# Performance work log

Hardware: AMD Instinct MI355X
Metric: run time of the kernel (lower is better)

## Reference

```python
import jax, jax.numpy as jnp
import numpy as np

N = 100000      # n_nodes
E = 1600000     # n_edges (avg degree 16)
F_IN = 128      # feat_dim
F_OUT = 128     # hid_dim


def setup_inputs() -> dict:
    key = jax.random.key(0)
    k1, k2, k3, k4 = jax.random.split(key, 4)
    x = jax.random.normal(k1, (N, F_IN), dtype=jnp.float32)
    edge_index = jax.random.randint(k2, (2, E), 0, N, dtype=jnp.int32)
    edge_weight = jax.random.uniform(k3, (E,), dtype=jnp.float32)
    # GCNConv level-0 parameters (Glorot-ish weight, zero bias as PyG default init)
    W = jax.random.normal(k4, (F_IN, F_OUT), dtype=jnp.float32) / np.sqrt(F_IN).astype(np.float32)
    b = jnp.zeros((F_OUT,), dtype=jnp.float32)
    return {"x": x, "W": W, "b": b, "level": 0,
            "edge_index": edge_index, "edge_weight": edge_weight}


def reference(x, W, b, level, edge_index, edge_weight):
    # PyG GCNConv: h = D^-1/2 (A + I) D^-1/2 (x @ W) + b ; Encoder also returns relu(h)
    n = x.shape[0]
    h = x @ W                                          # [N, F_OUT]
    src, dst = edge_index[0], edge_index[1]
    loop = jnp.arange(n, dtype=src.dtype)
    src = jnp.concatenate([src, loop])                 # add self-loops (weight 1)
    dst = jnp.concatenate([dst, loop])
    w = jnp.concatenate([edge_weight, jnp.ones((n,), edge_weight.dtype)])
    deg = jax.ops.segment_sum(w, dst, num_segments=n)  # in-degree by weight
    dinv = jnp.where(deg > 0, jax.lax.rsqrt(deg), 0.0)
    norm = dinv[src] * w * dinv[dst]                   # [E+N]
    emb = jax.ops.segment_sum(h[src] * norm[:, None], dst, num_segments=n) + b
    return emb, jax.nn.relu(emb)
```

## Files before the change

kernel.cpp:

```cpp
#include <hip/hip_runtime.h>

#define F 128
#define BSH 7
#define BWIDTH (1 << BSH)
#define MAX_NBKT 1024
#define CHUNK 4096
#define CAP 3072

typedef unsigned int uint;
typedef unsigned short ushort;

typedef __attribute__((ext_vector_type(8))) short bf16x8;
typedef __attribute__((ext_vector_type(4))) float f32x4;

union U4B8 { uint4 u; bf16x8 v; };

static __device__ inline ushort f2bf(float f) {
    uint u = __float_as_uint(f);
    return (ushort)((u + 0x7FFF + ((u >> 16) & 1)) >> 16);
}
static __device__ inline float bf2f(ushort h) {
    return __uint_as_float((uint)h << 16);
}

__global__ __launch_bounds__(256) void packW_kernel(const float* __restrict__ W,
                                                    uint4* __restrict__ wphi,
                                                    uint4* __restrict__ wplo,
                                                    int* __restrict__ gcur, int nbkt) {
    int idx = blockIdx.x * 256 + threadIdx.x;
    if (idx < nbkt) gcur[idx] = 0;
    if (idx >= 8 * 4 * 64) return;
    int l = idx & 63;
    int s = (idx >> 6) & 3;
    int t = idx >> 8;
    int p = t >> 1, q = t & 1;
    int col = 32 * p + 2 * (l & 15) + q;
    int kbase = 32 * s + (l >> 4) * 8;
    uint hi[8], lo[8];
    #pragma unroll
    for (int j = 0; j < 8; ++j) {
        float w = W[(size_t)(kbase + j) * F + col];
        ushort h = f2bf(w);
        lo[j] = f2bf(w - bf2f(h));
        hi[j] = h;
    }
    uint4 vh, vl;
    vh.x = hi[0] | (hi[1] << 16); vh.y = hi[2] | (hi[3] << 16);
    vh.z = hi[4] | (hi[5] << 16); vh.w = hi[6] | (hi[7] << 16);
    vl.x = lo[0] | (lo[1] << 16); vl.y = lo[2] | (lo[3] << 16);
    vl.z = lo[4] | (lo[5] << 16); vl.w = lo[6] | (lo[7] << 16);
    wphi[idx] = vh;
    wplo[idx] = vl;
}

__global__ __launch_bounds__(256) void scatter1_kernel(const int* __restrict__ src,
                                                       const int* __restrict__ dst,
                                                       const float* __restrict__ w,
                                                       int* __restrict__ gcur,
                                                       int2* __restrict__ ebuf,
                                                       int nbkt, int e) {
    __shared__ int hist[MAX_NBKT];
    __shared__ int cursor[MAX_NBKT];
    int t = threadIdx.x, blk = blockIdx.x;
    for (int i = t; i < nbkt; i += 256) hist[i] = 0;
    __syncthreads();
    int b0 = blk * CHUNK;
    #pragma unroll
    for (int j = 0; j < 16; ++j) {
        int i = b0 + t + 256 * j;
        if (i < e) atomicAdd(&hist[dst[i] >> BSH], 1);
    }
    __syncthreads();
    for (int i = t; i < nbkt; i += 256) {
        int c = hist[i];
        cursor[i] = c ? atomicAdd(&gcur[i], c) : 0;
    }
    __syncthreads();
    #pragma unroll
    for (int j = 0; j < 16; ++j) {
        int i = b0 + t + 256 * j;
        if (i < e) {
            int d = dst[i];
            int bk = d >> BSH;
            int pos = atomicAdd(&cursor[bk], 1);
            if (pos > CAP - 1) pos = CAP - 1;
            ebuf[(size_t)bk * CAP + pos] = make_int2(src[i] | ((d & (BWIDTH - 1)) << 17),
                                                     __float_as_int(w[i]));
        }
    }
}

__global__ __launch_bounds__(256) void bucket_build_kernel(int2* __restrict__ ebuf,
                                                           const int* __restrict__ gcur,
                                                           int2* __restrict__ rowinfo,
                                                           float* __restrict__ dinv,
                                                           int n, int nbkt) {
    __shared__ int2 stage[CAP];
    __shared__ int cnt[BWIDTH];
    __shared__ uint ws[BWIDTH];
    __shared__ float dvl[BWIDTH];
    __shared__ int cur[BWIDTH];
    __shared__ int offsh[BWIDTH];
    int b = blockIdx.x, t = threadIdx.x;
    size_t r0 = (size_t)b * CAP;
    int m = gcur[b];
    if (m > CAP) m = CAP;
    if (t < BWIDTH) { cnt[t] = 0; ws[t] = 0u; }
    __syncthreads();
    for (int i = t; i < m; i += 256) {
        int2 ed = ebuf[r0 + i];
        stage[i] = ed;
        int bl = (ed.x >> 17) & (BWIDTH - 1);
        atomicAdd(&cnt[bl], 1);
        atomicAdd(&ws[bl], (uint)(__int_as_float(ed.y) * 16777216.0f));
    }
    __syncthreads();
    if (t < BWIDTH) offsh[t] = cnt[t];
    __syncthreads();
    for (int off = 1; off < BWIDTH; off <<= 1) {
        int u = 0;
        if (t < BWIDTH && t >= off) u = offsh[t - off];
        __syncthreads();
        if (t < BWIDTH) offsh[t] += u;
        __syncthreads();
    }
    if (t < BWIDTH) {
        int excl = offsh[t] - cnt[t];
        cur[t] = excl;
        float dv = rsqrtf(1.0f + (float)ws[t] * (1.0f / 16777216.0f));
        dvl[t] = dv;
        int d = (b << BSH) + t;
        if (d < n) {
            rowinfo[d] = make_int2((int)(r0 + excl), cnt[t]);
            dinv[d] = dv;
        }
    }
    __syncthreads();
    for (int i = t; i < m; i += 256) {
        int2 ed = stage[i];
        int bl = (ed.x >> 17) & (BWIDTH - 1);
        int pos = atomicAdd(&cur[bl], 1);
        ebuf[r0 + pos] = make_int2(ed.x & 0x1FFFF,
                                   __float_as_int(__int_as_float(ed.y) * dvl[bl]));
    }
}

#define XPAD 136

__global__ __launch_bounds__(256) void gemm_kernel(const float* __restrict__ x,
                                                   const uint4* __restrict__ wphi,
                                                   const uint4* __restrict__ wplo,
                                                   ushort* __restrict__ hb, int n) {
    __shared__ ushort xhi[64][XPAD];
    __shared__ ushort xlo[64][XPAD];
    int row0 = blockIdx.x * 64;
    int t = threadIdx.x;
    #pragma unroll
    for (int i = 0; i < 8; ++i) {
        int v = t + 256 * i;
        int r = v >> 5, c4 = v & 31;
        int row = row0 + r;
        float4 val = (row < n) ? ((const float4*)x)[(size_t)row * 32 + c4]
                               : make_float4(0.f, 0.f, 0.f, 0.f);
        ushort h0 = f2bf(val.x), h1 = f2bf(val.y), h2 = f2bf(val.z), h3 = f2bf(val.w);
        ushort l0 = f2bf(val.x - bf2f(h0)), l1 = f2bf(val.y - bf2f(h1));
        ushort l2 = f2bf(val.z - bf2f(h2)), l3 = f2bf(val.w - bf2f(h3));
        *(ushort4*)&xhi[r][c4 * 4] = make_ushort4(h0, h1, h2, h3);
        *(ushort4*)&xlo[r][c4 * 4] = make_ushort4(l0, l1, l2, l3);
    }
    __syncthreads();

    int wv = t >> 6, l = t & 63;
    int m = l & 15, quad = l >> 4;
    f32x4 acc[8];
    #pragma unroll
    for (int i = 0; i < 8; ++i) acc[i] = (f32x4){0.f, 0.f, 0.f, 0.f};

    #pragma unroll
    for (int s = 0; s < 4; ++s) {
        bf16x8 ahi = *(const bf16x8*)&xhi[16 * wv + m][32 * s + quad * 8];
        bf16x8 alo = *(const bf16x8*)&xlo[16 * wv + m][32 * s + quad * 8];
        #pragma unroll
        for (int tt = 0; tt < 8; ++tt) {
            int widx = (tt * 4 + s) * 64 + l;
            U4B8 bh, bl;
            bh.u = wphi[widx];
            bl.u = wplo[widx];
            acc[tt] = __builtin_amdgcn_mfma_f32_16x16x32_bf16(ahi, bh.v, acc[tt], 0, 0, 0);
            acc[tt] = __builtin_amdgcn_mfma_f32_16x16x32_bf16(alo, bh.v, acc[tt], 0, 0, 0);
            acc[tt] = __builtin_amdgcn_mfma_f32_16x16x32_bf16(ahi, bl.v, acc[tt], 0, 0, 0);
        }
    }

    #pragma unroll
    for (int r = 0; r < 4; ++r) {
        int row = row0 + 16 * wv + quad * 4 + r;
        if (row < n) {
            uint* outp = (uint*)hb + (size_t)row * 64;
            #pragma unroll
            for (int p = 0; p < 4; ++p) {
                uint vp = (uint)f2bf(acc[2 * p][r]) | ((uint)f2bf(acc[2 * p + 1][r]) << 16);
                outp[p * 16 + m] = vp;
            }
        }
    }
}

__global__ __launch_bounds__(256) void aggregate_kernel(
        const ushort* __restrict__ hb, const int2* __restrict__ rowinfo,
        const int2* __restrict__ csr, const float* __restrict__ dinv,
        const float* __restrict__ b,
        float* __restrict__ out_emb, float* __restrict__ out_relu, int n) {
    int wave = threadIdx.x >> 6;
    int lane = threadIdx.x & 63;
    int i = blockIdx.x * 4 + wave;
    if (i >= n) return;
    int2 ri = rowinfo[i];
    int lo = ri.x, hi = ri.x + ri.y;
    float di = dinv[i];
    const uint* h32 = (const uint*)hb;
    uint hvu = h32[(size_t)i * 64 + lane];
    float2 bv = ((const float2*)b)[lane];
    float2 acc;
    acc.x = fmaf(__uint_as_float(hvu << 16) * di, di, bv.x);
    acc.y = fmaf(__uint_as_float(hvu & 0xFFFF0000u) * di, di, bv.y);
    for (int c = lo; c < hi; c += 64) {
        int m = min(64, hi - c);
        int sv = 0, nvi = 0;
        if (lane < m) {
            int2 en = csr[c + lane];
            sv = en.x;
            nvi = __float_as_int(__int_as_float(en.y) * dinv[sv]);
        }
        int mp = (m + 7) & ~7;
        for (int j = 0; j < mp; j += 8) {
            int ss[8]; float nw[8]; uint g[8];
            #pragma unroll
            for (int u = 0; u < 8; ++u) {
                ss[u] = __builtin_amdgcn_readlane(sv, j + u);
                nw[u] = __uint_as_float((uint)__builtin_amdgcn_readlane(nvi, j + u));
            }
            #pragma unroll
            for (int u = 0; u < 8; ++u)
                g[u] = h32[(size_t)ss[u] * 64 + lane];
            #pragma unroll
            for (int u = 0; u < 8; ++u) {
                acc.x = fmaf(__uint_as_float(g[u] << 16), nw[u], acc.x);
                acc.y = fmaf(__uint_as_float(g[u] & 0xFFFF0000u), nw[u], acc.y);
            }
        }
    }
    ((float2*)out_emb)[(size_t)i * 64 + lane] = acc;
    ((float2*)out_relu)[(size_t)i * 64 + lane] =
        make_float2(fmaxf(acc.x, 0.f), fmaxf(acc.y, 0.f));
}

extern "C" void kernel_launch(void* const* d_in, const int* in_sizes, int n_in,
                              void* d_out, int out_size, void* d_ws, size_t ws_size,
                              hipStream_t stream) {
    const float* x  = (const float*)d_in[0];
    const float* W  = (const float*)d_in[1];
    const float* b  = (const float*)d_in[2];
    const int*   ei = (const int*)d_in[4];
    const float* ew = (const float*)d_in[5];

    int n = in_sizes[0] / F;
    int e = in_sizes[4] / 2;
    const int* src = ei;
    const int* dst = ei + e;

    float* out_emb  = (float*)d_out;
    float* out_relu = out_emb + (size_t)n * F;

    int nbkt = (n + BWIDTH - 1) >> BSH;
    int eb   = (e + CHUNK - 1) / CHUNK;

    ushort* hb      = (ushort*)d_ws;
    int2*   ebuf    = (int2*)(hb + (size_t)n * F);
    uint4*  wphi    = (uint4*)(ebuf + (size_t)nbkt * CAP);
    uint4*  wplo    = wphi + 2048;
    int*    gcur    = (int*)(wplo + 2048);
    int2*   rowinfo = (int2*)(gcur + nbkt + 2);
    float*  dinv    = (float*)(rowinfo + n);

    packW_kernel<<<8, 256, 0, stream>>>(W, wphi, wplo, gcur, nbkt);
    scatter1_kernel<<<eb, 256, 0, stream>>>(src, dst, ew, gcur, ebuf, nbkt, e);
    bucket_build_kernel<<<nbkt, 256, 0, stream>>>(ebuf, gcur, rowinfo, dinv, n, nbkt);
    gemm_kernel<<<(n + 63) / 64, 256, 0, stream>>>(x, wphi, wplo, hb, n);
    aggregate_kernel<<<(n + 3) / 4, 256, 0, stream>>>(hb, rowinfo, ebuf, dinv, b,
                                                      out_emb, out_relu, n);
}
```

Before: 299.9 us.

## Locally sort edges per block before scattering and pad bucket counters

The edge scatter kernel now does a block-local counting sort in shared memory, with an exclusive scan over bucket histograms. It then writes edges to global memory in sorted order, so each bucket's writes are contiguous and coalesced rather than randomly scattered. Global bucket cursors are padded to 16 ints apart to reduce atomic contention and false sharing. The chunk is halved to 2048 edges to fit the shared staging buffers, which doubles the number of blocks and the count of global atomics.

```diff
diff --git a/kernel.cpp b/kernel.cpp
--- a/kernel.cpp
+++ b/kernel.cpp
@@ -4,8 +4,9 @@
 #define BSH 7
 #define BWIDTH (1 << BSH)
 #define MAX_NBKT 1024
-#define CHUNK 4096
+#define CHUNK 2048
 #define CAP 3072
+#define GPAD 16
 
 typedef unsigned int uint;
 typedef unsigned short ushort;
@@ -28,7 +29,7 @@
                                                     uint4* __restrict__ wplo,
                                                     int* __restrict__ gcur, int nbkt) {
     int idx = blockIdx.x * 256 + threadIdx.x;
-    if (idx < nbkt) gcur[idx] = 0;
+    for (int z = idx; z < nbkt * GPAD; z += 2048) gcur[z] = 0;
     if (idx >= 8 * 4 * 64) return;
     int l = idx & 63;
     int s = (idx >> 6) & 3;
@@ -60,34 +61,69 @@
                                                        int2* __restrict__ ebuf,
                                                        int nbkt, int e) {
     __shared__ int hist[MAX_NBKT];
+    __shared__ int shift[MAX_NBKT];
     __shared__ int cursor[MAX_NBKT];
+    __shared__ int2 sorted[CHUNK];
+    __shared__ int outaddr[CHUNK];
+    __shared__ int scanbuf[256];
     int t = threadIdx.x, blk = blockIdx.x;
     for (int i = t; i < nbkt; i += 256) hist[i] = 0;
     __syncthreads();
     int b0 = blk * CHUNK;
-    #pragma unroll
-    for (int j = 0; j < 16; ++j) {
+    int mtot = min(CHUNK, e - b0);
+    #pragma unroll
+    for (int j = 0; j < 8; ++j) {
         int i = b0 + t + 256 * j;
         if (i < e) atomicAdd(&hist[dst[i] >> BSH], 1);
     }
     __syncthreads();
-    for (int i = t; i < nbkt; i += 256) {
-        int c = hist[i];
-        cursor[i] = c ? atomicAdd(&gcur[i], c) : 0;
-    }
-    __syncthreads();
-    #pragma unroll
-    for (int j = 0; j < 16; ++j) {
+    int b4 = t * 4;
+    int h0 = 0, h1 = 0, h2 = 0, h3 = 0;
+    if (b4 < nbkt)     h0 = hist[b4];
+    if (b4 + 1 < nbkt) h1 = hist[b4 + 1];
+    if (b4 + 2 < nbkt) h2 = hist[b4 + 2];
+    if (b4 + 3 < nbkt) h3 = hist[b4 + 3];
+    int sum = h0 + h1 + h2 + h3;
+    scanbuf[t] = sum;
+    __syncthreads();
+    for (int off = 1; off < 256; off <<= 1) {
+        int u = (t >= off) ? scanbuf[t - off] : 0;
+        __syncthreads();
+        scanbuf[t] += u;
+        __syncthreads();
+    }
+    int excl = scanbuf[t] - sum;
+    int ls[4] = { excl, excl + h0, excl + h0 + h1, excl + h0 + h1 + h2 };
+    int hs[4] = { h0, h1, h2, h3 };
+    #pragma unroll
+    for (int q = 0; q < 4; ++q) {
+        int i = b4 + q;
+        if (i < nbkt) {
+            int c = hs[q];
+            int res = c ? atomicAdd(&gcur[i * GPAD], c) : 0;
+            cursor[i] = ls[q];
+            shift[i] = i * CAP + res - ls[q];
+        }
+    }
+    __syncthreads();
+    #pragma unroll
+    for (int j = 0; j < 8; ++j) {
         int i = b0 + t + 256 * j;
         if (i < e) {
             int d = dst[i];
             int bk = d >> BSH;
             int pos = atomicAdd(&cursor[bk], 1);
-            if (pos > CAP - 1) pos = CAP - 1;
-            ebuf[(size_t)bk * CAP + pos] = make_int2(src[i] | ((d & (BWIDTH - 1)) << 17),
-                                                     __float_as_int(w[i]));
-        }
-    }
+            int a = shift[bk] + pos;
+            int amax = bk * CAP + (CAP - 1);
+            if (a > amax) a = amax;
+            sorted[pos] = make_int2(src[i] | ((d & (BWIDTH - 1)) << 17),
+                                    __float_as_int(w[i]));
+            outaddr[pos] = a;
+        }
+    }
+    __syncthreads();
+    for (int i = t; i < mtot; i += 256)
+        ebuf[outaddr[i]] = sorted[i];
 }
 
 __global__ __launch_bounds__(256) void bucket_build_kernel(int2* __restrict__ ebuf,
@@ -103,7 +139,7 @@
     __shared__ int offsh[BWIDTH];
     int b = blockIdx.x, t = threadIdx.x;
     size_t r0 = (size_t)b * CAP;
-    int m = gcur[b];
+    int m = gcur[b * GPAD];
     if (m > CAP) m = CAP;
     if (t < BWIDTH) { cnt[t] = 0; ws[t] = 0u; }
     __syncthreads();
@@ -280,7 +316,7 @@
     uint4*  wphi    = (uint4*)(ebuf + (size_t)nbkt * CAP);
     uint4*  wplo    = wphi + 2048;
     int*    gcur    = (int*)(wplo + 2048);
-    int2*   rowinfo = (int2*)(gcur + nbkt + 2);
+    int2*   rowinfo = (int2*)(gcur + nbkt * GPAD + 2);
     float*  dinv    = (float*)(rowinfo + n);
 
     packW_kernel<<<8, 256, 0, stream>>>(W, wphi, wplo, gcur, nbkt);
```

Result: no change. 304.4 us (+1.5%).
